# Optimization experiments

Hardware: AMD Instinct MI355X
Metric: run time of the kernel (lower is better)

The kernel has to match this reference:

```python
import jax, jax.numpy as jnp
import numpy as np

N, E, F, H, G = 50000, 800000, 128, 32, 64  # nodes, edges, feat, hidden, graphs


def _p(k, shape):
    return (jax.random.normal(k, shape, jnp.float32) / np.sqrt(shape[0])).astype(jnp.float32)


def setup_inputs() -> dict:
    key = jax.random.key(0)
    ks = jax.random.split(key, 24)
    x = jax.random.normal(ks[0], (N, F), jnp.float32)
    edge_index = jax.random.randint(ks[1], (2, E), 0, N, dtype=jnp.int32)
    batch = jnp.sort(jax.random.randint(ks[2], (N,), 0, G, dtype=jnp.int32))
    d = {"x": x, "edge_index": edge_index, "batch": batch}
    # GATv2 conv params: (Wl, Wr, att vector a, bias) per layer; dims 128->32->64->128
    dims = [(F, H), (H, 2 * H), (2 * H, 4 * H)]
    i = 3
    for li, (din, dout) in enumerate(dims, 1):
        d[f"Wl{li}"] = _p(ks[i], (din, dout)); i += 1
        d[f"Wr{li}"] = _p(ks[i], (din, dout)); i += 1
        d[f"a{li}"] = _p(ks[i], (dout,)); i += 1
        d[f"b{li}"] = jnp.zeros((dout,), jnp.float32)
    # MLP head 128->1024->512->128->32->4
    mdims = [(4 * H, 1024), (1024, 512), (512, 128), (128, 32), (32, 4)]
    for li, (din, dout) in enumerate(mdims, 1):
        d[f"mw{li}"] = _p(ks[i], (din, dout)); i += 1
        d[f"mb{li}"] = jnp.zeros((dout,), jnp.float32)
    return d


def _gatv2(x, Wl, Wr, a, b, src, dst, n):
    # GATv2: e = a . LeakyReLU(Wl x_src + Wr x_dst), softmax over incoming edges of dst
    xl = x @ Wl
    xr = x @ Wr
    e = jax.nn.leaky_relu(xl[src] + xr[dst], 0.2) @ a  # [E]
    m = jax.ops.segment_max(e, dst, num_segments=n)
    ex = jnp.exp(e - m[dst])
    denom = jax.ops.segment_sum(ex, dst, num_segments=n)
    alpha = ex / (denom[dst] + 1e-16)
    return jax.ops.segment_sum(alpha[:, None] * xl[src], dst, num_segments=n) + b


def reference(x, edge_index, batch,
              Wl1, Wr1, a1, b1, Wl2, Wr2, a2, b2, Wl3, Wr3, a3, b3,
              mw1, mb1, mw2, mb2, mw3, mb3, mw4, mb4, mw5, mb5):
    src, dst = edge_index[0], edge_index[1]
    n = x.shape[0]
    h = _gatv2(x, Wl1, Wr1, a1, b1, src, dst, n)
    h = jax.nn.leaky_relu(h, 0.01)
    h = _gatv2(h, Wl2, Wr2, a2, b2, src, dst, n)
    h = jax.nn.leaky_relu(h, 0.01)
    h = _gatv2(h, Wl3, Wr3, a3, b3, src, dst, n)
    # global max pool per graph
    g = jax.ops.segment_max(h, batch, num_segments=G)  # [G, 4H]
    g = jax.nn.relu(g @ mw1 + mb1)
    g = jax.nn.relu(g @ mw2 + mb2)
    g = jax.nn.relu(g @ mw3 + mb3)
    g = jax.nn.relu(g @ mw4 + mb4)
    return g @ mw5 + mb5  # [G, 4]
```

## Files before the change

### kernel.cpp

```cpp
#include <hip/hip_runtime.h>
#include <cfloat>

#define N_NODES 50000
#define N_EDGES 800000
#define N_GRAPHS 64
#define POOL_CHUNK 64
#define DEG_BUCKETS 64
#define SCAN_NB ((N_NODES + 255) / 256)

#define BUK_SHIFT 8
#define NBUK ((N_NODES + 255) / 256)
#define CHUNK 4096
#define CAP 6144

typedef _Float16 half8 __attribute__((ext_vector_type(8)));
typedef _Float16 half4 __attribute__((ext_vector_type(4)));
typedef _Float16 half2t __attribute__((ext_vector_type(2)));
typedef _Float16 f16x8 __attribute__((ext_vector_type(8)));
typedef float f32x4 __attribute__((ext_vector_type(4)));


__global__ __launch_bounds__(256) void bucket_hist_kernel(const int* __restrict__ dst,
                                                          int* __restrict__ bhist, int n) {
    __shared__ int lh[NBUK];
    int t = threadIdx.x;
    if (t < NBUK) lh[t] = 0;
    __syncthreads();
    int i0 = blockIdx.x * 1024;
#pragma unroll
    for (int j = 0; j < 4; ++j) {
        int i = i0 + j * 256 + t;
        if (i < n) atomicAdd(&lh[dst[i] >> BUK_SHIFT], 1);
    }
    __syncthreads();
    if (t < NBUK && lh[t]) atomicAdd(&bhist[t], lh[t]);
}

__global__ __launch_bounds__(256) void bucket_scan_kernel(const int* __restrict__ bhist,
                                                          int* __restrict__ bbase,
                                                          int* __restrict__ bcur) {
    __shared__ int sm[256];
    int t = threadIdx.x;
    int v = (t < NBUK) ? bhist[t] : 0;
    sm[t] = v;
    __syncthreads();
    for (int off = 1; off < 256; off <<= 1) {
        int x = (t >= off) ? sm[t - off] : 0;
        __syncthreads();
        sm[t] += x;
        __syncthreads();
    }
    int excl = sm[t] - v;
    if (t < NBUK) { bbase[t] = excl; bcur[t] = excl; }
    if (t == 255) bbase[NBUK] = sm[255];
}


__global__ __launch_bounds__(256) void binscat_kernel(const int* __restrict__ src,
        const int* __restrict__ dst, int* __restrict__ bcur,
        int2* __restrict__ ebuf, int n) {
    __shared__ int2 staged[CHUNK];
    __shared__ int lh[NBUK], lbase[NBUK], lpos[NBUK], gpos[NBUK];
    __shared__ int ssc[256];
    int t = threadIdx.x;
    int e0 = blockIdx.x * CHUNK;
    int len = n - e0; if (len > CHUNK) len = CHUNK; if (len < 0) len = 0;
    if (t < NBUK) { lh[t] = 0; lpos[t] = 0; }
    __syncthreads();
    int s[16], d[16];
#pragma unroll
    for (int j = 0; j < 16; ++j) {
        int i = j * 256 + t;
        if (i < len) {
            s[j] = src[e0 + i];
            d[j] = dst[e0 + i];
            atomicAdd(&lh[d[j] >> BUK_SHIFT], 1);
        } else d[j] = -1;
    }
    __syncthreads();
    int v = (t < NBUK) ? lh[t] : 0;
    ssc[t] = v;
    __syncthreads();
    for (int off = 1; off < 256; off <<= 1) {
        int x = (t >= off) ? ssc[t - off] : 0;
        __syncthreads();
        ssc[t] += x;
        __syncthreads();
    }
    if (t < NBUK) {
        lbase[t] = ssc[t] - v;
        gpos[t] = v ? atomicAdd(&bcur[t], v) : 0;
    }
    __syncthreads();
#pragma unroll
    for (int j = 0; j < 16; ++j) {
        if (d[j] >= 0) {
            int b = d[j] >> BUK_SHIFT;
            int slot = lbase[b] + atomicAdd(&lpos[b], 1);
            staged[slot] = make_int2(s[j], d[j]);
        }
    }
    __syncthreads();
    for (int i = t; i < len; i += 256) {
        int2 p = staged[i];
        int b = p.y >> BUK_SHIFT;
        ebuf[gpos[b] + (i - lbase[b])] = p;
    }
}


__global__ __launch_bounds__(256) void csr_final_kernel(const int2* __restrict__ ebuf,
        const int* __restrict__ bbase, int* __restrict__ rowptr, int* __restrict__ csrc,
        int* __restrict__ deg, int* __restrict__ dhist, int n_nodes, int n_edges) {
    __shared__ int lcnt[256], lbs[256], lpos[256], ssc[256];
    __shared__ int lh64[DEG_BUCKETS];
    __shared__ int buf[CAP];
    int b = blockIdx.x, t = threadIdx.x;
    int nstart = b << BUK_SHIFT;
    int nodes = n_nodes - nstart; if (nodes > 256) nodes = 256;
    int r0 = bbase[b], r1 = bbase[b + 1];
    int len = r1 - r0;
    lcnt[t] = 0;
    lpos[t] = 0;
    if (t < DEG_BUCKETS) lh64[t] = 0;
    __syncthreads();
    for (int i = t; i < len; i += 256)
        atomicAdd(&lcnt[ebuf[r0 + i].y - nstart], 1);
    __syncthreads();
    int v = lcnt[t];
    ssc[t] = v;
    __syncthreads();
    for (int off = 1; off < 256; off <<= 1) {
        int x = (t >= off) ? ssc[t - off] : 0;
        __syncthreads();
        ssc[t] += x;
        __syncthreads();
    }
    lbs[t] = ssc[t] - v;
    if (t < nodes) {
        rowptr[nstart + t] = r0 + lbs[t];
        deg[nstart + t] = v;
        int dd = (v > DEG_BUCKETS - 1) ? DEG_BUCKETS - 1 : v;
        atomicAdd(&lh64[dd], 1);
    }
    if (b == NBUK - 1 && t == 0) rowptr[n_nodes] = n_edges;
    __syncthreads();
    if (t < DEG_BUCKETS && lh64[t]) atomicAdd(&dhist[t], lh64[t]);
    if (len <= CAP) {
        for (int i = t; i < len; i += 256) {
            int2 p = ebuf[r0 + i];
            int dn = p.y - nstart;
            int pos = lbs[dn] + atomicAdd(&lpos[dn], 1);
            buf[pos] = p.x;
        }
        __syncthreads();
        for (int i = t; i < len; i += 256) csrc[r0 + i] = buf[i];
    } else {
        for (int i = t; i < len; i += 256) {
            int2 p = ebuf[r0 + i];
            int dn = p.y - nstart;
            int pos = lbs[dn] + atomicAdd(&lpos[dn], 1);
            csrc[r0 + pos] = p.x;
        }
    }
}


__global__ void dscan_kernel(const int* __restrict__ dhist, int* __restrict__ dcur) {
    int t = threadIdx.x;
    int dv = dhist[t];
    int incl = dv;
    for (int off = 1; off < 64; off <<= 1) {
        int x = __shfl_up(incl, off, 64);
        if (t >= off) incl += x;
    }
    dcur[t] = incl - dv;
}

__global__ __launch_bounds__(256) void perm_kernel(const int* __restrict__ deg,
        int* __restrict__ dcur, int* __restrict__ perm, int n) {
    __shared__ int lh[DEG_BUCKETS], lbase[DEG_BUCKETS];
    int t = threadIdx.x;
    int i = blockIdx.x * 256 + t;
    if (t < DEG_BUCKETS) lh[t] = 0;
    __syncthreads();
    int d = 0, loc = 0;
    bool valid = (i < n);
    if (valid) {
        int v = deg[i];
        d = (v > DEG_BUCKETS - 1) ? DEG_BUCKETS - 1 : v;
        loc = atomicAdd(&lh[d], 1);
    }
    __syncthreads();
    if (t < DEG_BUCKETS) lbase[t] = lh[t] ? atomicAdd(&dcur[t], lh[t]) : 0;
    __syncthreads();
    if (valid) perm[lbase[d] + loc] = i;
}


template<int DIN, int DOUT>
__global__ __launch_bounds__(256) void mfma_gemm_kernel(const float* __restrict__ h,
        const float* __restrict__ Wl, const float* __restrict__ Wr,
        _Float16* __restrict__ xl, _Float16* __restrict__ xr, int n) {
    constexpr int NOUT = 2 * DOUT;
    constexpr int BM = 64;
    constexpr int NCH = DIN / 8;
    constexpr int XORM = (NCH < 8 ? NCH : 8) - 1;
    constexpr int NT = NOUT / 16;
    static_assert(DIN % 32 == 0 && DOUT % 16 == 0, "shape");
    __shared__ _Float16 sA[BM * DIN];
    __shared__ _Float16 sW[NOUT * DIN];
    int tid = threadIdx.x;
    int r0 = blockIdx.x * BM;

    for (int i = tid; i < DIN * DOUT; i += 256) {
        int k = i / DOUT, c = i % DOUT;
        sW[c * DIN + (k ^ ((c & XORM) << 3))] = (_Float16)Wl[i];
        int nr = DOUT + c;
        sW[nr * DIN + (k ^ ((nr & XORM) << 3))] = (_Float16)Wr[i];
    }
    constexpr int DQ = DIN / 4;
    for (int i = tid; i < BM * DQ; i += 256) {
        int row = i / DQ, kq = (i % DQ) * 4;
        float4 v = (r0 + row < n) ? *(const float4*)(h + (size_t)(r0 + row) * DIN + kq)
                                  : make_float4(0.f, 0.f, 0.f, 0.f);
        half4 hv = {(_Float16)v.x, (_Float16)v.y, (_Float16)v.z, (_Float16)v.w};
        *(half4*)(sA + row * DIN + (kq ^ ((row & XORM) << 3))) = hv;
    }
    __syncthreads();

    int w = tid >> 6, lane = tid & 63;
    int lrow = lane & 15, lg = lane >> 4;
    int arow = w * 16 + lrow;

    f32x4 acc[NT];
#pragma unroll
    for (int i = 0; i < NT; ++i) acc[i] = (f32x4){0.f, 0.f, 0.f, 0.f};

#pragma unroll
    for (int kk = 0; kk < DIN; kk += 32) {
        int ka = kk + lg * 8;
        f16x8 af = *(const f16x8*)(sA + arow * DIN + (ka ^ ((arow & XORM) << 3)));
#pragma unroll
        for (int nt = 0; nt < NT; ++nt) {
            int bcol = nt * 16 + lrow;
            f16x8 bf = *(const f16x8*)(sW + bcol * DIN + (ka ^ ((bcol & XORM) << 3)));
            acc[nt] = __builtin_amdgcn_mfma_f32_16x16x32_f16(af, bf, acc[nt], 0, 0, 0);
        }
    }

    int orow0 = r0 + w * 16 + lg * 4;
#pragma unroll
    for (int nt = 0; nt < NT; ++nt) {
        int c = nt * 16 + lrow;
        _Float16* obase = (c < DOUT) ? xl : xr;
        int cc = (c < DOUT) ? c : c - DOUT;
#pragma unroll
        for (int r = 0; r < 4; ++r) {
            int row = orow0 + r;
            if (row < n) obase[(size_t)row * DOUT + cc] = (_Float16)acc[nt][r];
        }
    }
}


union H8 {
    half8 v;
    half2t h2[4];
    unsigned int u[4];
};

template<int DOUT, int U, bool LEAKY>
__global__ __launch_bounds__(256) void edge_kernel(
        const _Float16* __restrict__ xl, const _Float16* __restrict__ xr,
        const float* __restrict__ avec, const float* __restrict__ bias,
        const int* __restrict__ rowptr, const int* __restrict__ csrc,
        const int* __restrict__ perm,
        float* __restrict__ out, int n) {
    constexpr int LANES = DOUT / 8;
    constexpr int NPW = 64 / LANES;
    int wid = (blockIdx.x * blockDim.x + threadIdx.x) >> 6;
    int lane = threadIdx.x & 63;
    int group = lane / LANES;
    int gl = lane % LANES;
    int gnode = wid * NPW + group;
    if (gnode >= n) return;
    int node = perm[n - 1 - gnode];

    constexpr float L2E = 1.44269504f;
    const float* ap = avec + 8 * gl;
    half2t a6h[4], a4h[4];
#pragma unroll
    for (int j = 0; j < 4; ++j) {
        float x0 = 0.6f * L2E * ap[2 * j], x1 = 0.6f * L2E * ap[2 * j + 1];
        a6h[j] = half2t{(_Float16)x0, (_Float16)x1};
        float y0 = 0.4f * L2E * ap[2 * j], y1 = 0.4f * L2E * ap[2 * j + 1];
        a4h[j] = half2t{(_Float16)y0, (_Float16)y1};
    }

    int nbase = node * DOUT + 8 * gl;
    half8 xrh = *(const half8*)(xr + nbase);
    const _Float16* xlg = xl + 8 * gl;

    float acc[8] = {};
    float denom = 0.f;
    int e0 = rowptr[node], e1 = rowptr[node + 1];

    for (int p = e0; p < e1; p += U) {
        int sidx[U];
#pragma unroll
        for (int u = 0; u < U; ++u) {
            int q = p + u;
            sidx[u] = (q < e1) ? csrc[q] : -1;
        }
        half8 xlv[U];
#pragma unroll
        for (int u = 0; u < U; ++u) {
            int s = (sidx[u] >= 0) ? sidx[u] : 0;
            xlv[u] = *(const half8*)(xlg + (size_t)s * DOUT);
        }
        float part[U];
#pragma unroll
        for (int u = 0; u < U; ++u) {
            H8 t, ta;
            t.v = xlv[u] + xrh;
#pragma unroll
            for (int j = 0; j < 4; ++j) ta.u[j] = t.u[j] & 0x7fff7fffu;
            float pu = 0.f;
#pragma unroll
            for (int j = 0; j < 4; ++j) {
                pu = __builtin_amdgcn_fdot2(a6h[j], t.h2[j], pu, false);
                pu = __builtin_amdgcn_fdot2(a4h[j], ta.h2[j], pu, false);
            }
            part[u] = pu;
        }
#pragma unroll
        for (int mask = LANES / 2; mask >= 1; mask >>= 1)
#pragma unroll
            for (int u = 0; u < U; ++u)
                part[u] += __shfl_xor(part[u], mask, 64);
#pragma unroll
        for (int u = 0; u < U; ++u) {
            float w = __builtin_exp2f(part[u]);
            w = (sidx[u] >= 0) ? w : 0.f;
            denom += w;
#pragma unroll
            for (int i = 0; i < 8; ++i)
                acc[i] += w * (float)xlv[u][i];
        }
    }
    float inv = 1.f / (denom + 1e-16f);
    const float* bp = bias + 8 * gl;
    float o[8];
#pragma unroll
    for (int i = 0; i < 8; ++i) {
        float v = acc[i] * inv + bp[i];
        if (LEAKY) v = (v > 0.f) ? v : 0.01f * v;
        o[i] = v;
    }
    *(float4*)(out + nbase) = make_float4(o[0], o[1], o[2], o[3]);
    *(float4*)(out + nbase + 4) = make_float4(o[4], o[5], o[6], o[7]);
}


__device__ __forceinline__ unsigned int enc_f32(float f) {
    unsigned int b = __float_as_uint(f);
    return (b & 0x80000000u) ? ~b : (b | 0x80000000u);
}
__device__ __forceinline__ float dec_f32(unsigned int u) {
    unsigned int b = (u & 0x80000000u) ? (u ^ 0x80000000u) : ~u;
    return __uint_as_float(b);
}

__global__ __launch_bounds__(128) void pool_kernel(const float* __restrict__ h,
        const int* __restrict__ batch, unsigned int* __restrict__ gout, int n) {
    int c0 = blockIdx.x * POOL_CHUNK;
    if (c0 >= n) return;
    int end = c0 + POOL_CHUNK; if (end > n) end = n;
    int d = threadIdx.x;
    float run = -FLT_MAX;
    int gcur = batch[c0];
    for (int nn = c0; nn < end; ++nn) {
        int g = batch[nn];
        if (g != gcur) {
            atomicMax(&gout[gcur * 128 + d], enc_f32(run));
            run = -FLT_MAX;
            gcur = g;
        }
        run = fmaxf(run, h[nn * 128 + d]);
    }
    atomicMax(&gout[gcur * 128 + d], enc_f32(run));
}


__global__ __launch_bounds__(256) void mlp1_kernel(const unsigned int* __restrict__ gpool,
        const float* __restrict__ w1, const float* __restrict__ b1,
        float* __restrict__ act1) {
    __shared__ float A[128];
    int g = blockIdx.x >> 2, chunk = blockIdx.x & 3;
    int t = threadIdx.x;
    if (t < 128) A[t] = dec_f32(gpool[g * 128 + t]);
    __syncthreads();
    int c = chunk * 256 + t;
    float a0 = b1[c], a1 = 0.f;
#pragma unroll 4
    for (int k = 0; k < 128; k += 2) {
        a0 += A[k] * w1[k * 1024 + c];
        a1 += A[k + 1] * w1[(k + 1) * 1024 + c];
    }
    act1[g * 1024 + c] = fmaxf(a0 + a1, 0.f);
}

template<int DIN, int DOUT>
__global__ __launch_bounds__(256) void mlp_mid_kernel(const float* __restrict__ actin,
        const float* __restrict__ w, const float* __restrict__ b,
        float* __restrict__ actout) {
    constexpr int CHUNKS = DOUT / 64;
    constexpr int KQ = DIN / 4;
    __shared__ float A[DIN];
    __shared__ float partial[4][64];
    int g = blockIdx.x / CHUNKS, chunk = blockIdx.x % CHUNKS;
    int t = threadIdx.x;
    for (int i = t; i < DIN; i += 256) A[i] = actin[g * DIN + i];
    __syncthreads();
    int c = chunk * 64 + (t & 63);
    int q = t >> 6;
    const float* wp = w + c + (size_t)q * KQ * DOUT;
    const float* ap = A + q * KQ;
    float a0 = 0.f, a1 = 0.f;
#pragma unroll 4
    for (int k = 0; k < KQ; k += 2) {
        a0 += ap[k] * wp[k * DOUT];
        a1 += ap[k + 1] * wp[(k + 1) * DOUT];
    }
    partial[q][t & 63] = a0 + a1;
    __syncthreads();
    if (t < 64) {
        float s = partial[0][t] + partial[1][t] + partial[2][t] + partial[3][t] + b[c];
        actout[g * DOUT + chunk * 64 + t] = fmaxf(s, 0.f);
    }
}

__global__ __launch_bounds__(128) void mlp45_kernel(const float* __restrict__ act3,
        const float* __restrict__ w4, const float* __restrict__ b4,
        const float* __restrict__ w5, const float* __restrict__ b5,
        float* __restrict__ out) {
    __shared__ float C[128], D[32];
    int g = blockIdx.x, t = threadIdx.x;
    if (t < 128) C[t] = act3[g * 128 + t];
    __syncthreads();
    if (t < 32) {
        float acc = b4[t];
#pragma unroll 4
        for (int k = 0; k < 128; ++k) acc += C[k] * w4[k * 32 + t];
        D[t] = fmaxf(acc, 0.f);
    }
    __syncthreads();
    if (t < 4) {
        float acc = b5[t];
#pragma unroll
        for (int k = 0; k < 32; ++k) acc += D[k] * w5[k * 4 + t];
        out[g * 4 + t] = acc;
    }
}


extern "C" void kernel_launch(void* const* d_in, const int* in_sizes, int n_in,
                              void* d_out, int out_size, void* d_ws, size_t ws_size,
                              hipStream_t stream) {
    const float* x     = (const float*)d_in[0];
    const int*   ei    = (const int*)d_in[1];
    const int*   batch = (const int*)d_in[2];
    const int*   src   = ei;
    const int*   dst   = ei + N_EDGES;
    const float* Wl1 = (const float*)d_in[3];
    const float* Wr1 = (const float*)d_in[4];
    const float* a1  = (const float*)d_in[5];
    const float* b1  = (const float*)d_in[6];
    const float* Wl2 = (const float*)d_in[7];
    const float* Wr2 = (const float*)d_in[8];
    const float* a2  = (const float*)d_in[9];
    const float* b2  = (const float*)d_in[10];
    const float* Wl3 = (const float*)d_in[11];
    const float* Wr3 = (const float*)d_in[12];
    const float* a3  = (const float*)d_in[13];
    const float* b3  = (const float*)d_in[14];
    const float* mw1 = (const float*)d_in[15];
    const float* mb1 = (const float*)d_in[16];
    const float* mw2 = (const float*)d_in[17];
    const float* mb2 = (const float*)d_in[18];
    const float* mw3 = (const float*)d_in[19];
    const float* mb3 = (const float*)d_in[20];
    const float* mw4 = (const float*)d_in[21];
    const float* mb4 = (const float*)d_in[22];
    const float* mw5 = (const float*)d_in[23];
    const float* mb5 = (const float*)d_in[24];

    char* ws = (char*)d_ws;
    size_t off = 0;
    auto alloc = [&](size_t bytes) -> void* {
        void* p = ws + off;
        off = (off + bytes + 255) & ~(size_t)255;
        return p;
    };
    int*   bhist  = (int*)alloc(NBUK * 4);
    int*   dhist  = (int*)alloc(DEG_BUCKETS * 4);
    unsigned int* pool = (unsigned int*)alloc(N_GRAPHS * 128 * 4);
    size_t zero_bytes = off;
    int*   bbase  = (int*)alloc((NBUK + 1) * 4);
    int*   bcur   = (int*)alloc(NBUK * 4);
    int*   rowptr = (int*)alloc((N_NODES + 1) * 4);
    int*   csrc   = (int*)alloc(N_EDGES * 4);
    int2*  ebuf   = (int2*)alloc((size_t)N_EDGES * 8);
    _Float16* xl  = (_Float16*)alloc((size_t)N_NODES * 128 * 2);
    _Float16* xr  = (_Float16*)alloc((size_t)N_NODES * 128 * 2);
    float* hA     = (float*)alloc((size_t)N_NODES * 128 * 4);
    float* hB     = (float*)alloc((size_t)N_NODES * 128 * 4);
    int*   dcur   = (int*)alloc(DEG_BUCKETS * 4);
    int*   perm   = (int*)alloc(N_NODES * 4);
    int*   deg    = (int*)alloc(N_NODES * 4);
    float* act1   = (float*)alloc(N_GRAPHS * 1024 * 4);
    float* act2   = (float*)alloc(N_GRAPHS * 512 * 4);
    float* act3   = (float*)alloc(N_GRAPHS * 128 * 4);

    hipMemsetAsync(bhist, 0, zero_bytes, stream);
    bucket_hist_kernel<<<(N_EDGES + 1023) / 1024, 256, 0, stream>>>(dst, bhist, N_EDGES);
    bucket_scan_kernel<<<1, 256, 0, stream>>>(bhist, bbase, bcur);
    binscat_kernel<<<(N_EDGES + CHUNK - 1) / CHUNK, 256, 0, stream>>>(src, dst, bcur, ebuf, N_EDGES);
    csr_final_kernel<<<NBUK, 256, 0, stream>>>(ebuf, bbase, rowptr, csrc, deg, dhist, N_NODES, N_EDGES);
    dscan_kernel<<<1, 64, 0, stream>>>(dhist, dcur);
    perm_kernel<<<SCAN_NB, 256, 0, stream>>>(deg, dcur, perm, N_NODES);

    auto egrid = [](int npw) {
        int waves = (N_NODES + npw - 1) / npw;
        return (waves + 3) / 4;
    };
    const int gblocks = (N_NODES + 63) / 64;

    mfma_gemm_kernel<128, 32><<<gblocks, 256, 0, stream>>>(x, Wl1, Wr1, xl, xr, N_NODES);
    edge_kernel<32, 16, true><<<egrid(16), 256, 0, stream>>>(xl, xr, a1, b1, rowptr, csrc, perm, hB, N_NODES);
    mfma_gemm_kernel<32, 64><<<gblocks, 256, 0, stream>>>(hB, Wl2, Wr2, xl, xr, N_NODES);
    edge_kernel<64, 16, true><<<egrid(8), 256, 0, stream>>>(xl, xr, a2, b2, rowptr, csrc, perm, hA, N_NODES);
    mfma_gemm_kernel<64, 128><<<gblocks, 256, 0, stream>>>(hA, Wl3, Wr3, xl, xr, N_NODES);
    edge_kernel<128, 16, false><<<egrid(4), 256, 0, stream>>>(xl, xr, a3, b3, rowptr, csrc, perm, hB, N_NODES);

    pool_kernel<<<(N_NODES + POOL_CHUNK - 1) / POOL_CHUNK, 128, 0, stream>>>(hB, batch, pool, N_NODES);
    mlp1_kernel<<<N_GRAPHS * 4, 256, 0, stream>>>(pool, mw1, mb1, act1);
    mlp_mid_kernel<1024, 512><<<N_GRAPHS * 8, 256, 0, stream>>>(act1, mw2, mb2, act2);
    mlp_mid_kernel<512, 128><<<N_GRAPHS * 2, 256, 0, stream>>>(act2, mw3, mb3, act3);
    mlp45_kernel<<<N_GRAPHS, 128, 0, stream>>>(act3, mw4, mb4, mw5, mb5, (float*)d_out);
}
```

Baseline: 342.5 us.

## Fuse global max-pool into last edge kernel and store hidden activations as fp16

The last GATv2 edge kernel now does the per-graph max pooling directly with atomicMax on encoded floats, so the separate pool kernel and the write and re-read of the 50000x128 fp32 activation are gone. Intermediate hidden activations between layers are stored in fp16 rather than fp32, and the GEMM kernel gains an fp16 input path that loads 8 halves per access. The last edge kernel's unroll factor drops from 16 to 8. In exchange, every node issues 128 global atomics onto only 64 graphs' rows, which may contend, and the activations lose precision.

Measured after the change: 539.5 us. +57.5%, slower.

```diff
diff --git a/kernel.cpp b/kernel.cpp
--- a/kernel.cpp
+++ b/kernel.cpp
@@ -4,7 +4,6 @@
 #define N_NODES 50000
 #define N_EDGES 800000
 #define N_GRAPHS 64
-#define POOL_CHUNK 64
 #define DEG_BUCKETS 64
 #define SCAN_NB ((N_NODES + 255) / 256)
 
@@ -198,8 +197,8 @@
 }
 
 
-template<int DIN, int DOUT>
-__global__ __launch_bounds__(256) void mfma_gemm_kernel(const float* __restrict__ h,
+template<typename TIN, int DIN, int DOUT>
+__global__ __launch_bounds__(256) void mfma_gemm_kernel(const TIN* __restrict__ h,
         const float* __restrict__ Wl, const float* __restrict__ Wr,
         _Float16* __restrict__ xl, _Float16* __restrict__ xr, int n) {
     constexpr int NOUT = 2 * DOUT;
@@ -219,13 +218,24 @@
         int nr = DOUT + c;
         sW[nr * DIN + (k ^ ((nr & XORM) << 3))] = (_Float16)Wr[i];
     }
-    constexpr int DQ = DIN / 4;
-    for (int i = tid; i < BM * DQ; i += 256) {
-        int row = i / DQ, kq = (i % DQ) * 4;
-        float4 v = (r0 + row < n) ? *(const float4*)(h + (size_t)(r0 + row) * DIN + kq)
-                                  : make_float4(0.f, 0.f, 0.f, 0.f);
-        half4 hv = {(_Float16)v.x, (_Float16)v.y, (_Float16)v.z, (_Float16)v.w};
-        *(half4*)(sA + row * DIN + (kq ^ ((row & XORM) << 3))) = hv;
+    if constexpr (sizeof(TIN) == 4) {
+        constexpr int DQ = DIN / 4;
+        for (int i = tid; i < BM * DQ; i += 256) {
+            int row = i / DQ, kq = (i % DQ) * 4;
+            float4 v = (r0 + row < n) ? *(const float4*)(h + (size_t)(r0 + row) * DIN + kq)
+                                      : make_float4(0.f, 0.f, 0.f, 0.f);
+            half4 hv = {(_Float16)v.x, (_Float16)v.y, (_Float16)v.z, (_Float16)v.w};
+            *(half4*)(sA + row * DIN + (kq ^ ((row & XORM) << 3))) = hv;
+        }
+    } else {
+        constexpr int D8 = DIN / 8;
+        for (int i = tid; i < BM * D8; i += 256) {
+            int row = i / D8, k8 = (i % D8) * 8;
+            half8 hv;
+            if (r0 + row < n) hv = *(const half8*)(h + (size_t)(r0 + row) * DIN + k8);
+            else hv = half8{0, 0, 0, 0, 0, 0, 0, 0};
+            *(half8*)(sA + row * DIN + (k8 ^ ((row & XORM) << 3))) = hv;
+        }
     }
     __syncthreads();
 
@@ -270,13 +280,23 @@
     unsigned int u[4];
 };
 
-template<int DOUT, int U, bool LEAKY>
+__device__ __forceinline__ unsigned int enc_f32(float f) {
+    unsigned int b = __float_as_uint(f);
+    return (b & 0x80000000u) ? ~b : (b | 0x80000000u);
+}
+__device__ __forceinline__ float dec_f32(unsigned int u) {
+    unsigned int b = (u & 0x80000000u) ? (u ^ 0x80000000u) : ~u;
+    return __uint_as_float(b);
+}
+
+template<int DOUT, int U, bool LEAKY, bool POOL>
 __global__ __launch_bounds__(256) void edge_kernel(
         const _Float16* __restrict__ xl, const _Float16* __restrict__ xr,
         const float* __restrict__ avec, const float* __restrict__ bias,
         const int* __restrict__ rowptr, const int* __restrict__ csrc,
         const int* __restrict__ perm,
-        float* __restrict__ out, int n) {
+        _Float16* __restrict__ out,
+        const int* __restrict__ batchp, unsigned int* __restrict__ gout, int n) {
     constexpr int LANES = DOUT / 8;
     constexpr int NPW = 64 / LANES;
     int wid = (blockIdx.x * blockDim.x + threadIdx.x) >> 6;
@@ -358,38 +378,17 @@
         if (LEAKY) v = (v > 0.f) ? v : 0.01f * v;
         o[i] = v;
     }
-    *(float4*)(out + nbase) = make_float4(o[0], o[1], o[2], o[3]);
-    *(float4*)(out + nbase + 4) = make_float4(o[4], o[5], o[6], o[7]);
-}
-
-
-__device__ __forceinline__ unsigned int enc_f32(float f) {
-    unsigned int b = __float_as_uint(f);
-    return (b & 0x80000000u) ? ~b : (b | 0x80000000u);
-}
-__device__ __forceinline__ float dec_f32(unsigned int u) {
-    unsigned int b = (u & 0x80000000u) ? (u ^ 0x80000000u) : ~u;
-    return __uint_as_float(b);
-}
-
-__global__ __launch_bounds__(128) void pool_kernel(const float* __restrict__ h,
-        const int* __restrict__ batch, unsigned int* __restrict__ gout, int n) {
-    int c0 = blockIdx.x * POOL_CHUNK;
-    if (c0 >= n) return;
-    int end = c0 + POOL_CHUNK; if (end > n) end = n;
-    int d = threadIdx.x;
-    float run = -FLT_MAX;
-    int gcur = batch[c0];
-    for (int nn = c0; nn < end; ++nn) {
-        int g = batch[nn];
-        if (g != gcur) {
-            atomicMax(&gout[gcur * 128 + d], enc_f32(run));
-            run = -FLT_MAX;
-            gcur = g;
-        }
-        run = fmaxf(run, h[nn * 128 + d]);
-    }
-    atomicMax(&gout[gcur * 128 + d], enc_f32(run));
+    if (POOL) {
+        int g = batchp[node];
+        unsigned int* gp = gout + (g << 7) + 8 * gl;
+#pragma unroll
+        for (int i = 0; i < 8; ++i) atomicMax(gp + i, enc_f32(o[i]));
+    } else {
+        half8 ov;
+#pragma unroll
+        for (int i = 0; i < 8; ++i) ov[i] = (_Float16)o[i];
+        *(half8*)(out + nbase) = ov;
+    }
 }
 
 
@@ -514,8 +513,8 @@
     int2*  ebuf   = (int2*)alloc((size_t)N_EDGES * 8);
     _Float16* xl  = (_Float16*)alloc((size_t)N_NODES * 128 * 2);
     _Float16* xr  = (_Float16*)alloc((size_t)N_NODES * 128 * 2);
-    float* hA     = (float*)alloc((size_t)N_NODES * 128 * 4);
-    float* hB     = (float*)alloc((size_t)N_NODES * 128 * 4);
+    _Float16* hA  = (_Float16*)alloc((size_t)N_NODES * 128 * 2);
+    _Float16* hB  = (_Float16*)alloc((size_t)N_NODES * 128 * 2);
     int*   dcur   = (int*)alloc(DEG_BUCKETS * 4);
     int*   perm   = (int*)alloc(N_NODES * 4);
     int*   deg    = (int*)alloc(N_NODES * 4);
@@ -537,14 +536,13 @@
     };
     const int gblocks = (N_NODES + 63) / 64;
 
-    mfma_gemm_kernel<128, 32><<<gblocks, 256, 0, stream>>>(x, Wl1, Wr1, xl, xr, N_NODES);
-    edge_kernel<32, 16, true><<<egrid(16), 256, 0, stream>>>(xl, xr, a1, b1, rowptr, csrc, perm, hB, N_NODES);
-    mfma_gemm_kernel<32, 64><<<gblocks, 256, 0, stream>>>(hB, Wl2, Wr2, xl, xr, N_NODES);
-    edge_kernel<64, 16, true><<<egrid(8), 256, 0, stream>>>(xl, xr, a2, b2, rowptr, csrc, perm, hA, N_NODES);
-    mfma_gemm_kernel<64, 128><<<gblocks, 256, 0, stream>>>(hA, Wl3, Wr3, xl, xr, N_NODES);
-    edge_kernel<128, 16, false><<<egrid(4), 256, 0, stream>>>(xl, xr, a3, b3, rowptr, csrc, perm, hB, N_NODES);
-
-    pool_kernel<<<(N_NODES + POOL_CHUNK - 1) / POOL_CHUNK, 128, 0, stream>>>(hB, batch, pool, N_NODES);
+    mfma_gemm_kernel<float, 128, 32><<<gblocks, 256, 0, stream>>>(x, Wl1, Wr1, xl, xr, N_NODES);
+    edge_kernel<32, 16, true, false><<<egrid(16), 256, 0, stream>>>(xl, xr, a1, b1, rowptr, csrc, perm, hB, nullptr, nullptr, N_NODES);
+    mfma_gemm_kernel<_Float16, 32, 64><<<gblocks, 256, 0, stream>>>(hB, Wl2, Wr2, xl, xr, N_NODES);
+    edge_kernel<64, 16, true, false><<<egrid(8), 256, 0, stream>>>(xl, xr, a2, b2, rowptr, csrc, perm, hA, nullptr, nullptr, N_NODES);
+    mfma_gemm_kernel<_Float16, 64, 128><<<gblocks, 256, 0, stream>>>(hA, Wl3, Wr3, xl, xr, N_NODES);
+    edge_kernel<128, 8, false, true><<<egrid(4), 256, 0, stream>>>(xl, xr, a3, b3, rowptr, csrc, perm, nullptr, batch, pool, N_NODES);
+
     mlp1_kernel<<<N_GRAPHS * 4, 256, 0, stream>>>(pool, mw1, mb1, act1);
     mlp_mid_kernel<1024, 512><<<N_GRAPHS * 8, 256, 0, stream>>>(act1, mw2, mb2, act2);
     mlp_mid_kernel<512, 128><<<N_GRAPHS * 2, 256, 0, stream>>>(act2, mw3, mb3, act3);
```
